# Optimization experiments

Measured on AMD Instinct MI355X. Metric: run time of the kernel, lower is better.

The kernel has to match this reference:

```python
import jax, jax.numpy as jnp
import numpy as np

DIM = 512
HEADS = 8
DIM_HEAD = 64
INNER = HEADS * DIM_HEAD  # 512


def setup_inputs() -> dict:
    key = jax.random.key(0)
    ks = jax.random.split(key, 6)
    B, N = 8, 1024
    x = jax.random.normal(ks[0], (B, N, DIM), dtype=jnp.float32)
    w_qkv = jax.random.normal(ks[1], (DIM, 3 * INNER), dtype=jnp.float32) * (DIM ** -0.5)
    reattn_weights = jax.random.normal(ks[2], (HEADS, HEADS), dtype=jnp.float32)
    ln_gamma = jnp.ones((HEADS,), dtype=jnp.float32)
    ln_beta = jnp.zeros((HEADS,), dtype=jnp.float32)
    w_out = jax.random.normal(ks[3], (INNER, DIM), dtype=jnp.float32) * (INNER ** -0.5)
    b_out = jnp.zeros((DIM,), dtype=jnp.float32)
    return {"x": x, "w_qkv": w_qkv, "reattn_weights": reattn_weights,
            "ln_gamma": ln_gamma, "ln_beta": ln_beta, "w_out": w_out, "b_out": b_out}


def reference(x, w_qkv, reattn_weights, ln_gamma, ln_beta, w_out, b_out):
    B, N, C = x.shape
    scale = DIM_HEAD ** -0.5
    qkv = (x @ w_qkv).reshape(B, N, 3, HEADS, DIM_HEAD)
    qkv = jnp.transpose(qkv, (2, 0, 3, 1, 4))  # [3, B, H, N, D]
    q, k, v = qkv[0], qkv[1], qkv[2]
    dots = jnp.einsum('bhid,bhjd->bhij', q, k) * scale
    attn = jax.nn.softmax(dots, axis=-1)
    # cross-head re-mixing
    attn = jnp.einsum('bhij,hg->bgij', attn, reattn_weights)
    # LayerNorm over the head axis per (b, i, j)
    mean = jnp.mean(attn, axis=1, keepdims=True)
    var = jnp.var(attn, axis=1, keepdims=True)
    attn = (attn - mean) * jax.lax.rsqrt(var + 1e-5)
    attn = attn * ln_gamma[None, :, None, None] + ln_beta[None, :, None, None]
    out = jnp.einsum('bhij,bhjd->bhid', attn, v)
    out = jnp.transpose(out, (0, 2, 1, 3)).reshape(B, N, INNER)
    return out @ w_out + b_out
```

## Files before the change

kernel.cpp:

```cpp
#include <hip/hip_runtime.h>
#include <hip/hip_bf16.h>
#include <stdint.h>


#define DIMC 512

typedef __attribute__((ext_vector_type(8))) short bf16x8;
typedef __attribute__((ext_vector_type(4))) float f32x4;
typedef __attribute__((ext_vector_type(8))) unsigned short u16x8;

__device__ __forceinline__ unsigned short f2bf(float f) {
    union { float f; uint32_t u; } v; v.f = f;
    uint32_t u = v.u;
    return (unsigned short)((u + 0x7fffu + ((u >> 16) & 1u)) >> 16);
}

#define MFMA(a, b, c) __builtin_amdgcn_mfma_f32_16x16x32_bf16((a), (b), (c), 0, 0, 0)

#define GLOAD16(gptr, lptr)                                                        \
    __builtin_amdgcn_global_load_lds((const __attribute__((address_space(1))) void*)(gptr), \
                                     (__attribute__((address_space(3))) void*)(lptr), 16, 0, 0)

__global__ void k_conv(const float* __restrict__ in, unsigned short* __restrict__ out, int n8) {
    int t = blockIdx.x * blockDim.x + threadIdx.x;
    if (t >= n8) return;
    const float4* p = reinterpret_cast<const float4*>(in) + (size_t)t * 2;
    float4 a = p[0], b = p[1];
    u16x8 o;
    o[0] = f2bf(a.x); o[1] = f2bf(a.y); o[2] = f2bf(a.z); o[3] = f2bf(a.w);
    o[4] = f2bf(b.x); o[5] = f2bf(b.y); o[6] = f2bf(b.z); o[7] = f2bf(b.w);
    *(reinterpret_cast<u16x8*>(out) + t) = o;
}

__global__ __launch_bounds__(256) void k_tconv(const float* __restrict__ in,
                                               unsigned short* __restrict__ out, int R, int C) {
    __shared__ float tile[64][65];
    int ct = C >> 6;
    int bx = blockIdx.x % ct;
    int by = blockIdx.x / ct;
    int r0 = by * 64, c0 = bx * 64;
    int tx = threadIdx.x & 63, ty = threadIdx.x >> 6;
#pragma unroll
    for (int rr = 0; rr < 16; rr++) {
        int row = ty + rr * 4;
        tile[row][tx] = in[(size_t)(r0 + row) * C + c0 + tx];
    }
    __syncthreads();
#pragma unroll
    for (int rr = 0; rr < 16; rr++) {
        int row = ty + rr * 4;
        out[(size_t)(c0 + row) * R + r0 + tx] = f2bf(tile[tx][row]);
    }
}

__global__ __launch_bounds__(256) void k_qkv(const unsigned short* __restrict__ A,
                                             const unsigned short* __restrict__ BT,
                                             unsigned short* __restrict__ q,
                                             unsigned short* __restrict__ kk,
                                             unsigned short* __restrict__ vv) {
    __shared__ unsigned short Al[128 * 32];
    __shared__ unsigned short Bl[128 * 32];
    int mt = blockIdx.x / 12, nt = blockIdx.x % 12;
    int m0 = mt * 128, c0 = nt * 128;
    int tid = threadIdx.x, lane = tid & 63, w = tid >> 6;
    int wr = w >> 1, wc = w & 1;
    int lr = lane & 15, lb = lane >> 4;
    f32x4 acc[4][4] = {};
    const unsigned short* gA = A + (size_t)(m0 + 32 * w + (lane >> 2)) * DIMC + (lane & 3) * 8;
    const unsigned short* gB = BT + (size_t)(c0 + 32 * w + (lane >> 2)) * DIMC + (lane & 3) * 8;
    char* lA = (char*)Al + w * 2048;
    char* lB = (char*)Bl + w * 2048;
    for (int k0 = 0; k0 < DIMC; k0 += 32) {
        __syncthreads();
        GLOAD16(gA + k0, lA);
        GLOAD16(gA + k0 + 16 * DIMC, lA + 1024);
        GLOAD16(gB + k0, lB);
        GLOAD16(gB + k0 + 16 * DIMC, lB + 1024);
        __syncthreads();
        bf16x8 af[4], bfr[4];
#pragma unroll
        for (int mi = 0; mi < 4; mi++)
            af[mi] = *reinterpret_cast<const bf16x8*>(&Al[(64 * wr + 16 * mi + lr) * 32 + 8 * lb]);
#pragma unroll
        for (int ni = 0; ni < 4; ni++)
            bfr[ni] = *reinterpret_cast<const bf16x8*>(&Bl[(64 * wc + 16 * ni + lr) * 32 + 8 * lb]);
#pragma unroll
        for (int mi = 0; mi < 4; mi++)
#pragma unroll
            for (int ni = 0; ni < 4; ni++)
                acc[mi][ni] = MFMA(af[mi], bfr[ni], acc[mi][ni]);
    }
#pragma unroll
    for (int ni = 0; ni < 4; ni++) {
        int c = c0 + 64 * wc + 16 * ni + lr;
        int which = c >> 9, rem = c & 511, h = rem >> 6, d = rem & 63;
        unsigned short* dst = which == 0 ? q : (which == 1 ? kk : vv);
        float sc = which == 0 ? 0.125f : 1.0f;
#pragma unroll
        for (int mi = 0; mi < 4; mi++) {
#pragma unroll
            for (int r = 0; r < 4; r++) {
                int m = m0 + 64 * wr + 16 * mi + 4 * lb + r;
                int b = m >> 10, n = m & 1023;
                dst[(((size_t)(b * 8 + h) * 1024) + n) * 64 + d] = f2bf(acc[mi][ni][r] * sc);
            }
        }
    }
}

__global__ __launch_bounds__(256) void k_vtrans(const unsigned short* __restrict__ v,
                                                unsigned short* __restrict__ vT) {
    __shared__ unsigned short tile[64][72];
    int bh = blockIdx.x >> 4;
    int n0 = (blockIdx.x & 15) * 64;
    int t = threadIdx.x;
    int nl = t >> 2, c4 = t & 3;
    const u16x8* src = reinterpret_cast<const u16x8*>(v + ((size_t)bh * 1024 + n0 + nl) * 64 + c4 * 16);
    u16x8 x0 = src[0], x1 = src[1];
    *reinterpret_cast<u16x8*>(&tile[nl][c4 * 16]) = x0;
    *reinterpret_cast<u16x8*>(&tile[nl][c4 * 16 + 8]) = x1;
    __syncthreads();
    int dl = t >> 2, n4 = t & 3;
#pragma unroll
    for (int c = 0; c < 2; c++) {
        u16x8 o;
#pragma unroll
        for (int i = 0; i < 8; i++) o[i] = tile[n4 * 16 + 8 * c + i][dl];
        *reinterpret_cast<u16x8*>(vT + ((size_t)bh * 64 + dl) * 1024 + n0 + n4 * 16 + 8 * c) = o;
    }
}

__global__ __launch_bounds__(512) void k_attn(const unsigned short* __restrict__ q,
                                              const unsigned short* __restrict__ kk,
                                              unsigned short* __restrict__ P) {
    __shared__ float redm[32][8];
    __shared__ float redl[32][8];
    int blk = blockIdx.x;
    int bh = blk & 63, it = blk >> 6;
    int i0 = it * 32;
    int tid = threadIdx.x, w = tid >> 6, lane = tid & 63;
    int lr = lane & 15, lb = lane >> 4;
    int j0 = w * 128;
    const unsigned short* qp = q + (size_t)bh * 65536;
    const unsigned short* kp = kk + (size_t)bh * 65536;
    bf16x8 aq[2][2];
#pragma unroll
    for (int mf = 0; mf < 2; mf++)
#pragma unroll
        for (int ks = 0; ks < 2; ks++)
            aq[mf][ks] = *reinterpret_cast<const bf16x8*>(qp + (size_t)(i0 + 16 * mf + lr) * 64 + 32 * ks + 8 * lb);
    f32x4 acc[2][8] = {};
#pragma unroll
    for (int nf = 0; nf < 8; nf++) {
#pragma unroll
        for (int ks = 0; ks < 2; ks++) {
            bf16x8 bk = *reinterpret_cast<const bf16x8*>(kp + (size_t)(j0 + 16 * nf + lr) * 64 + 32 * ks + 8 * lb);
            acc[0][nf] = MFMA(aq[0][ks], bk, acc[0][nf]);
            acc[1][nf] = MFMA(aq[1][ks], bk, acc[1][nf]);
        }
    }
    float mfin[2][4];
#pragma unroll
    for (int mf = 0; mf < 2; mf++)
#pragma unroll
        for (int r = 0; r < 4; r++) {
            float m = acc[mf][0][r];
#pragma unroll
            for (int nf = 1; nf < 8; nf++) m = fmaxf(m, acc[mf][nf][r]);
            m = fmaxf(m, __shfl_xor(m, 1)); m = fmaxf(m, __shfl_xor(m, 2));
            m = fmaxf(m, __shfl_xor(m, 4)); m = fmaxf(m, __shfl_xor(m, 8));
            mfin[mf][r] = m;
        }
    if (lr == 0) {
#pragma unroll
        for (int mf = 0; mf < 2; mf++)
#pragma unroll
            for (int r = 0; r < 4; r++) redm[16 * mf + 4 * lb + r][w] = mfin[mf][r];
    }
    __syncthreads();
#pragma unroll
    for (int mf = 0; mf < 2; mf++)
#pragma unroll
        for (int r = 0; r < 4; r++) {
            int row = 16 * mf + 4 * lb + r;
            float m = redm[row][0];
#pragma unroll
            for (int ww = 1; ww < 8; ww++) m = fmaxf(m, redm[row][ww]);
            mfin[mf][r] = m;
        }
    float lfin[2][4];
#pragma unroll
    for (int mf = 0; mf < 2; mf++)
#pragma unroll
        for (int r = 0; r < 4; r++) {
            float s = 0.f;
#pragma unroll
            for (int nf = 0; nf < 8; nf++) {
                float e = __expf(acc[mf][nf][r] - mfin[mf][r]);
                acc[mf][nf][r] = e;
                s += e;
            }
            s += __shfl_xor(s, 1); s += __shfl_xor(s, 2);
            s += __shfl_xor(s, 4); s += __shfl_xor(s, 8);
            lfin[mf][r] = s;
        }
    if (lr == 0) {
#pragma unroll
        for (int mf = 0; mf < 2; mf++)
#pragma unroll
            for (int r = 0; r < 4; r++) redl[16 * mf + 4 * lb + r][w] = lfin[mf][r];
    }
    __syncthreads();
#pragma unroll
    for (int mf = 0; mf < 2; mf++)
#pragma unroll
        for (int r = 0; r < 4; r++) {
            int row = 16 * mf + 4 * lb + r;
            float s = 0.f;
#pragma unroll
            for (int ww = 0; ww < 8; ww++) s += redl[row][ww];
            lfin[mf][r] = 1.0f / s;
        }
    unsigned short* pp = P + (size_t)bh * 1048576;
#pragma unroll
    for (int mf = 0; mf < 2; mf++)
#pragma unroll
        for (int nf = 0; nf < 8; nf++)
#pragma unroll
            for (int r = 0; r < 4; r++)
                pp[(size_t)(i0 + 16 * mf + 4 * lb + r) * 1024 + j0 + 16 * nf + lr] =
                    f2bf(acc[mf][nf][r] * lfin[mf][r]);
}

__global__ __launch_bounds__(512) void k_mixpv(const unsigned short* __restrict__ P,
                                               const unsigned short* __restrict__ vT,
                                               const float* __restrict__ Wm,
                                               const float* __restrict__ gamma,
                                               const float* __restrict__ beta,
                                               unsigned short* __restrict__ outh) {
    __shared__ unsigned short Pex[8 * 1024];
    __shared__ unsigned short PMl[8 * 1024];
    int blk = blockIdx.x;
    int b = blk & 7, it = blk >> 3;
    int i0 = it * 16;
    int tid = threadIdx.x, w = tid >> 6, lane = tid & 63;
    int lr = lane & 15, lb = lane >> 4;
    float wv[64];
#pragma unroll
    for (int x2 = 0; x2 < 64; x2++) wv[x2] = Wm[x2];
    float cv[8];
#pragma unroll
    for (int h = 0; h < 8; h++) {
        float s = 0.f;
#pragma unroll
        for (int g = 0; g < 8; g++) s += wv[h * 8 + g];
        cv[h] = s * 0.125f;
    }
    float gv[8], bvv[8];
#pragma unroll
    for (int x2 = 0; x2 < 8; x2++) { gv[x2] = gamma[x2]; bvv[x2] = beta[x2]; }
    const unsigned short* pbase = P + (size_t)(b * 8 + w) * 1048576 + (size_t)i0 * 1024;
    const unsigned short* vp = vT + (size_t)(b * 8 + w) * 65536;
    int ii = tid >> 5;
    int jj = (tid & 31) * 2;
    f32x4 accO[4] = {};

    auto PH1 = [&](int jt) {
        int j0 = jt * 64;
#pragma unroll
        for (int c = 0; c < 2; c++) {
            int o = c * 512 + lane * 8;
            GLOAD16(pbase + (size_t)(o >> 6) * 1024 + j0 + (o & 63),
                    (char*)Pex + w * 2048 + c * 1024);
        }
    };
    auto PH2 = [&]() {
        float alo[8], ahi[8];
#pragma unroll
        for (int h = 0; h < 8; h++) {
            uint32_t pv = *reinterpret_cast<const uint32_t*>(Pex + h * 1024 + ii * 64 + jj);
            alo[h] = __uint_as_float(pv << 16);
            ahi[h] = __uint_as_float(pv & 0xffff0000u);
        }
        float mgl[8], mgh[8];
        float meanl = 0.f, meanh = 0.f;
#pragma unroll
        for (int g = 0; g < 8; g++) {
            float sl = 0.f, sh = 0.f;
#pragma unroll
            for (int h = 0; h < 8; h++) { sl += alo[h] * wv[h * 8 + g]; sh += ahi[h] * wv[h * 8 + g]; }
            mgl[g] = sl; mgh[g] = sh;
        }
#pragma unroll
        for (int h = 0; h < 8; h++) { meanl += alo[h] * cv[h]; meanh += ahi[h] * cv[h]; }
        float vl = 0.f, vh = 0.f;
#pragma unroll
        for (int g = 0; g < 8; g++) {
            float dl = mgl[g] - meanl, dh = mgh[g] - meanh;
            vl += dl * dl; vh += dh * dh;
        }
        float rl = rsqrtf(vl * 0.125f + 1e-5f), rh = rsqrtf(vh * 0.125f + 1e-5f);
#pragma unroll
        for (int g = 0; g < 8; g++) {
            unsigned short ol = f2bf((mgl[g] - meanl) * rl * gv[g] + bvv[g]);
            unsigned short oh = f2bf((mgh[g] - meanh) * rh * gv[g] + bvv[g]);
            uint32_t pk = (uint32_t)ol | ((uint32_t)oh << 16);
            int byteoff = (g * 2048 + ii * 128 + jj * 2) ^ ((ii & 7) << 4);
            *reinterpret_cast<uint32_t*>((char*)PMl + byteoff) = pk;
        }
    };
    auto PH3 = [&](int jt) {
        int j0 = jt * 64;
        bf16x8 Af[2];
#pragma unroll
        for (int kc = 0; kc < 2; kc++) {
            int byteoff = (w * 2048 + lr * 128 + kc * 64 + lb * 16) ^ ((lr & 7) << 4);
            Af[kc] = *reinterpret_cast<const bf16x8*>((const char*)PMl + byteoff);
        }
#pragma unroll
        for (int kc = 0; kc < 2; kc++)
#pragma unroll
            for (int df = 0; df < 4; df++) {
                bf16x8 bv8 = *reinterpret_cast<const bf16x8*>(vp + (size_t)(16 * df + lr) * 1024 + j0 + 32 * kc + 8 * lb);
                accO[df] = MFMA(Af[kc], bv8, accO[df]);
            }
    };

    PH1(0);
    __syncthreads();
    PH2();
    __syncthreads();
    for (int jt = 0; jt < 16; jt++) {
        if (jt < 15) PH1(jt + 1);
        PH3(jt);
        __syncthreads();
        if (jt < 15) PH2();
        __syncthreads();
    }
    int bi = b * 1024 + i0;
#pragma unroll
    for (int df = 0; df < 4; df++)
#pragma unroll
        for (int r = 0; r < 4; r++)
            outh[(size_t)(bi + 4 * lb + r) * 512 + w * 64 + 16 * df + lr] = f2bf(accO[df][r]);
}

__global__ __launch_bounds__(256) void k_proj(const unsigned short* __restrict__ A,
                                              const unsigned short* __restrict__ BT,
                                              const float* __restrict__ bias,
                                              float* __restrict__ out) {
    __shared__ unsigned short Al[128 * 32];
    __shared__ unsigned short Bl[128 * 32];
    int mt = blockIdx.x >> 2, nt = blockIdx.x & 3;
    int m0 = mt * 128, c0 = nt * 128;
    int tid = threadIdx.x, lane = tid & 63, w = tid >> 6;
    int wr = w >> 1, wc = w & 1;
    int lr = lane & 15, lb = lane >> 4;
    f32x4 acc[4][4] = {};
    const unsigned short* gA = A + (size_t)(m0 + 32 * w + (lane >> 2)) * DIMC + (lane & 3) * 8;
    const unsigned short* gB = BT + (size_t)(c0 + 32 * w + (lane >> 2)) * DIMC + (lane & 3) * 8;
    char* lA = (char*)Al + w * 2048;
    char* lB = (char*)Bl + w * 2048;
    for (int k0 = 0; k0 < DIMC; k0 += 32) {
        __syncthreads();
        GLOAD16(gA + k0, lA);
        GLOAD16(gA + k0 + 16 * DIMC, lA + 1024);
        GLOAD16(gB + k0, lB);
        GLOAD16(gB + k0 + 16 * DIMC, lB + 1024);
        __syncthreads();
        bf16x8 af[4], bfr[4];
#pragma unroll
        for (int mi = 0; mi < 4; mi++)
            af[mi] = *reinterpret_cast<const bf16x8*>(&Al[(64 * wr + 16 * mi + lr) * 32 + 8 * lb]);
#pragma unroll
        for (int ni = 0; ni < 4; ni++)
            bfr[ni] = *reinterpret_cast<const bf16x8*>(&Bl[(64 * wc + 16 * ni + lr) * 32 + 8 * lb]);
#pragma unroll
        for (int mi = 0; mi < 4; mi++)
#pragma unroll
            for (int ni = 0; ni < 4; ni++)
                acc[mi][ni] = MFMA(af[mi], bfr[ni], acc[mi][ni]);
    }
#pragma unroll
    for (int ni = 0; ni < 4; ni++) {
        int c = c0 + 64 * wc + 16 * ni + lr;
        float bs = bias[c];
#pragma unroll
        for (int mi = 0; mi < 4; mi++) {
#pragma unroll
            for (int r = 0; r < 4; r++) {
                int m = m0 + 64 * wr + 16 * mi + 4 * lb + r;
                out[(size_t)m * 512 + c] = acc[mi][ni][r] + bs;
            }
        }
    }
}

extern "C" void kernel_launch(void* const* d_in, const int* in_sizes, int n_in,
                              void* d_out, int out_size, void* d_ws, size_t ws_size,
                              hipStream_t stream) {
    (void)in_sizes; (void)n_in; (void)out_size; (void)ws_size;
    const float* x      = (const float*)d_in[0];
    const float* w_qkv  = (const float*)d_in[1];
    const float* W      = (const float*)d_in[2];
    const float* gamma  = (const float*)d_in[3];
    const float* beta   = (const float*)d_in[4];
    const float* w_out  = (const float*)d_in[5];
    const float* b_out  = (const float*)d_in[6];
    float* out = (float*)d_out;

    char* ws = (char*)d_ws;
    unsigned short* xb   = (unsigned short*)(ws + 0);
    unsigned short* wbT  = (unsigned short*)(ws + 8388608);
    unsigned short* w_oT = (unsigned short*)(ws + 9961472);
    unsigned short* q    = (unsigned short*)(ws + 10485760);
    unsigned short* k    = (unsigned short*)(ws + 18874368);
    unsigned short* v    = (unsigned short*)(ws + 27262976);
    unsigned short* vT   = (unsigned short*)(ws + 35651584);
    unsigned short* outh = (unsigned short*)(ws + 44040192);
    unsigned short* P    = (unsigned short*)(ws + 52428800);

    k_conv<<<2048, 256, 0, stream>>>(x, xb, 8192 * 512 / 8);
    k_tconv<<<(512 / 64) * (1536 / 64), 256, 0, stream>>>(w_qkv, wbT, 512, 1536);
    k_tconv<<<(512 / 64) * (512 / 64), 256, 0, stream>>>(w_out, w_oT, 512, 512);
    k_qkv<<<(8192 / 128) * (1536 / 128), 256, 0, stream>>>(xb, wbT, q, k, v);
    k_vtrans<<<64 * 16, 256, 0, stream>>>(v, vT);
    k_attn<<<64 * 32, 512, 0, stream>>>(q, k, P);
    k_mixpv<<<8 * 64, 512, 0, stream>>>(P, vT, W, gamma, beta, outh);
    k_proj<<<(8192 / 128) * (512 / 128), 256, 0, stream>>>(outh, w_oT, b_out, out);
}
```

Baseline: 260.5 us.

## Halve row tiles in attention and mix kernels, stage P stores via LDS

k_attn now handles 16 query rows per block instead of 32, doubling the grid, and stages the normalized probabilities through padded shared memory so each P row is written with 16-byte vector stores instead of scattered 2-byte stores. k_mixpv now processes 8 rows per block with one element per thread and doubles its grid; its MFMA still computes 16 rows, with half the output discarded. The aim is more blocks across the CUs and coalesced writes of the large P buffer, at the cost of wasted MFMA work in the mix kernel and re-reading K and V tiles per smaller block.

```diff
diff --git a/kernel.cpp b/kernel.cpp
--- a/kernel.cpp
+++ b/kernel.cpp
@@ -133,103 +133,90 @@
 __global__ __launch_bounds__(512) void k_attn(const unsigned short* __restrict__ q,
                                               const unsigned short* __restrict__ kk,
                                               unsigned short* __restrict__ P) {
-    __shared__ float redm[32][8];
-    __shared__ float redl[32][8];
+    __shared__ float redm[16][8];
+    __shared__ float redl[16][8];
+    __shared__ unsigned short stg[8][16 * 136];
     int blk = blockIdx.x;
     int bh = blk & 63, it = blk >> 6;
-    int i0 = it * 32;
+    int i0 = it * 16;
     int tid = threadIdx.x, w = tid >> 6, lane = tid & 63;
     int lr = lane & 15, lb = lane >> 4;
     int j0 = w * 128;
     const unsigned short* qp = q + (size_t)bh * 65536;
     const unsigned short* kp = kk + (size_t)bh * 65536;
-    bf16x8 aq[2][2];
-#pragma unroll
-    for (int mf = 0; mf < 2; mf++)
-#pragma unroll
-        for (int ks = 0; ks < 2; ks++)
-            aq[mf][ks] = *reinterpret_cast<const bf16x8*>(qp + (size_t)(i0 + 16 * mf + lr) * 64 + 32 * ks + 8 * lb);
-    f32x4 acc[2][8] = {};
+    bf16x8 aq[2];
+#pragma unroll
+    for (int ks = 0; ks < 2; ks++)
+        aq[ks] = *reinterpret_cast<const bf16x8*>(qp + (size_t)(i0 + lr) * 64 + 32 * ks + 8 * lb);
+    f32x4 acc[8] = {};
 #pragma unroll
     for (int nf = 0; nf < 8; nf++) {
 #pragma unroll
         for (int ks = 0; ks < 2; ks++) {
             bf16x8 bk = *reinterpret_cast<const bf16x8*>(kp + (size_t)(j0 + 16 * nf + lr) * 64 + 32 * ks + 8 * lb);
-            acc[0][nf] = MFMA(aq[0][ks], bk, acc[0][nf]);
-            acc[1][nf] = MFMA(aq[1][ks], bk, acc[1][nf]);
-        }
-    }
-    float mfin[2][4];
-#pragma unroll
-    for (int mf = 0; mf < 2; mf++)
-#pragma unroll
-        for (int r = 0; r < 4; r++) {
-            float m = acc[mf][0][r];
-#pragma unroll
-            for (int nf = 1; nf < 8; nf++) m = fmaxf(m, acc[mf][nf][r]);
-            m = fmaxf(m, __shfl_xor(m, 1)); m = fmaxf(m, __shfl_xor(m, 2));
-            m = fmaxf(m, __shfl_xor(m, 4)); m = fmaxf(m, __shfl_xor(m, 8));
-            mfin[mf][r] = m;
-        }
+            acc[nf] = MFMA(aq[ks], bk, acc[nf]);
+        }
+    }
+    float mx[4], li[4];
+#pragma unroll
+    for (int r = 0; r < 4; r++) {
+        float m = acc[0][r];
+#pragma unroll
+        for (int nf = 1; nf < 8; nf++) m = fmaxf(m, acc[nf][r]);
+        m = fmaxf(m, __shfl_xor(m, 1)); m = fmaxf(m, __shfl_xor(m, 2));
+        m = fmaxf(m, __shfl_xor(m, 4)); m = fmaxf(m, __shfl_xor(m, 8));
+        mx[r] = m;
+    }
     if (lr == 0) {
 #pragma unroll
-        for (int mf = 0; mf < 2; mf++)
-#pragma unroll
-            for (int r = 0; r < 4; r++) redm[16 * mf + 4 * lb + r][w] = mfin[mf][r];
-    }
-    __syncthreads();
-#pragma unroll
-    for (int mf = 0; mf < 2; mf++)
-#pragma unroll
-        for (int r = 0; r < 4; r++) {
-            int row = 16 * mf + 4 * lb + r;
-            float m = redm[row][0];
-#pragma unroll
-            for (int ww = 1; ww < 8; ww++) m = fmaxf(m, redm[row][ww]);
-            mfin[mf][r] = m;
-        }
-    float lfin[2][4];
-#pragma unroll
-    for (int mf = 0; mf < 2; mf++)
-#pragma unroll
-        for (int r = 0; r < 4; r++) {
-            float s = 0.f;
-#pragma unroll
-            for (int nf = 0; nf < 8; nf++) {
-                float e = __expf(acc[mf][nf][r] - mfin[mf][r]);
-                acc[mf][nf][r] = e;
-                s += e;
-            }
-            s += __shfl_xor(s, 1); s += __shfl_xor(s, 2);
-            s += __shfl_xor(s, 4); s += __shfl_xor(s, 8);
-            lfin[mf][r] = s;
-        }
+        for (int r = 0; r < 4; r++) redm[4 * lb + r][w] = mx[r];
+    }
+    __syncthreads();
+#pragma unroll
+    for (int r = 0; r < 4; r++) {
+        float m = redm[4 * lb + r][0];
+#pragma unroll
+        for (int ww = 1; ww < 8; ww++) m = fmaxf(m, redm[4 * lb + r][ww]);
+        mx[r] = m;
+    }
+#pragma unroll
+    for (int r = 0; r < 4; r++) {
+        float s = 0.f;
+#pragma unroll
+        for (int nf = 0; nf < 8; nf++) {
+            float e = __expf(acc[nf][r] - mx[r]);
+            acc[nf][r] = e;
+            s += e;
+        }
+        s += __shfl_xor(s, 1); s += __shfl_xor(s, 2);
+        s += __shfl_xor(s, 4); s += __shfl_xor(s, 8);
+        li[r] = s;
+    }
     if (lr == 0) {
 #pragma unroll
-        for (int mf = 0; mf < 2; mf++)
-#pragma unroll
-            for (int r = 0; r < 4; r++) redl[16 * mf + 4 * lb + r][w] = lfin[mf][r];
-    }
-    __syncthreads();
-#pragma unroll
-    for (int mf = 0; mf < 2; mf++)
-#pragma unroll
-        for (int r = 0; r < 4; r++) {
-            int row = 16 * mf + 4 * lb + r;
-            float s = 0.f;
-#pragma unroll
-            for (int ww = 0; ww < 8; ww++) s += redl[row][ww];
-            lfin[mf][r] = 1.0f / s;
-        }
+        for (int r = 0; r < 4; r++) redl[4 * lb + r][w] = li[r];
+    }
+    __syncthreads();
+#pragma unroll
+    for (int r = 0; r < 4; r++) {
+        float s = 0.f;
+#pragma unroll
+        for (int ww = 0; ww < 8; ww++) s += redl[4 * lb + r][ww];
+        li[r] = 1.0f / s;
+    }
+    unsigned short* sp = &stg[w][0];
+#pragma unroll
+    for (int nf = 0; nf < 8; nf++)
+#pragma unroll
+        for (int r = 0; r < 4; r++)
+            sp[(4 * lb + r) * 136 + 16 * nf + lr] = f2bf(acc[nf][r] * li[r]);
     unsigned short* pp = P + (size_t)bh * 1048576;
 #pragma unroll
-    for (int mf = 0; mf < 2; mf++)
-#pragma unroll
-        for (int nf = 0; nf < 8; nf++)
-#pragma unroll
-            for (int r = 0; r < 4; r++)
-                pp[(size_t)(i0 + 16 * mf + 4 * lb + r) * 1024 + j0 + 16 * nf + lr] =
-                    f2bf(acc[mf][nf][r] * lfin[mf][r]);
+    for (int ss = 0; ss < 4; ss++) {
+        int rowi = 4 * ss + lb;
+        u16x8 vv = *reinterpret_cast<const u16x8*>(&stg[w][rowi * 136 + lr * 8]);
+        *reinterpret_cast<u16x8*>(pp + (size_t)(i0 + rowi) * 1024 + j0 + lr * 8) = vv;
+    }
 }
 
 __global__ __launch_bounds__(512) void k_mixpv(const unsigned short* __restrict__ P,
@@ -238,11 +225,11 @@
                                                const float* __restrict__ gamma,
                                                const float* __restrict__ beta,
                                                unsigned short* __restrict__ outh) {
-    __shared__ unsigned short Pex[8 * 1024];
+    __shared__ unsigned short Pex[8 * 512];
     __shared__ unsigned short PMl[8 * 1024];
     int blk = blockIdx.x;
     int b = blk & 7, it = blk >> 3;
-    int i0 = it * 16;
+    int i0 = it * 8;
     int tid = threadIdx.x, w = tid >> 6, lane = tid & 63;
     int lr = lane & 15, lb = lane >> 4;
     float wv[64];
@@ -259,54 +246,43 @@
     float gv[8], bvv[8];
 #pragma unroll
     for (int x2 = 0; x2 < 8; x2++) { gv[x2] = gamma[x2]; bvv[x2] = beta[x2]; }
-    const unsigned short* pbase = P + (size_t)(b * 8 + w) * 1048576 + (size_t)i0 * 1024;
     const unsigned short* vp = vT + (size_t)(b * 8 + w) * 65536;
-    int ii = tid >> 5;
-    int jj = (tid & 31) * 2;
+    int e = tid * 8;
+    int sh = e >> 9, si = (e >> 6) & 7, sj = e & 63;
+    const unsigned short* psrc = P + (size_t)(b * 8 + sh) * 1048576 + (size_t)(i0 + si) * 1024 + sj;
+    int ii = tid >> 6, jj = tid & 63;
     f32x4 accO[4] = {};
 
     auto PH1 = [&](int jt) {
-        int j0 = jt * 64;
-#pragma unroll
-        for (int c = 0; c < 2; c++) {
-            int o = c * 512 + lane * 8;
-            GLOAD16(pbase + (size_t)(o >> 6) * 1024 + j0 + (o & 63),
-                    (char*)Pex + w * 2048 + c * 1024);
-        }
+        GLOAD16(psrc + jt * 64, (char*)Pex + tid * 16);
     };
     auto PH2 = [&]() {
-        float alo[8], ahi[8];
+        float av[8];
 #pragma unroll
         for (int h = 0; h < 8; h++) {
-            uint32_t pv = *reinterpret_cast<const uint32_t*>(Pex + h * 1024 + ii * 64 + jj);
-            alo[h] = __uint_as_float(pv << 16);
-            ahi[h] = __uint_as_float(pv & 0xffff0000u);
-        }
-        float mgl[8], mgh[8];
-        float meanl = 0.f, meanh = 0.f;
+            uint32_t pv = (uint32_t)Pex[h * 512 + ii * 64 + jj];
+            av[h] = __uint_as_float(pv << 16);
+        }
+        float mg[8];
+        float mean = 0.f;
 #pragma unroll
         for (int g = 0; g < 8; g++) {
-            float sl = 0.f, sh = 0.f;
-#pragma unroll
-            for (int h = 0; h < 8; h++) { sl += alo[h] * wv[h * 8 + g]; sh += ahi[h] * wv[h * 8 + g]; }
-            mgl[g] = sl; mgh[g] = sh;
-        }
-#pragma unroll
-        for (int h = 0; h < 8; h++) { meanl += alo[h] * cv[h]; meanh += ahi[h] * cv[h]; }
-        float vl = 0.f, vh = 0.f;
+            float s = 0.f;
+#pragma unroll
+            for (int h = 0; h < 8; h++) s += av[h] * wv[h * 8 + g];
+            mg[g] = s;
+        }
+#pragma unroll
+        for (int h = 0; h < 8; h++) mean += av[h] * cv[h];
+        float vvar = 0.f;
+#pragma unroll
+        for (int g = 0; g < 8; g++) { float d = mg[g] - mean; vvar += d * d; }
+        float rs = rsqrtf(vvar * 0.125f + 1e-5f);
 #pragma unroll
         for (int g = 0; g < 8; g++) {
-            float dl = mgl[g] - meanl, dh = mgh[g] - meanh;
-            vl += dl * dl; vh += dh * dh;
-        }
-        float rl = rsqrtf(vl * 0.125f + 1e-5f), rh = rsqrtf(vh * 0.125f + 1e-5f);
-#pragma unroll
-        for (int g = 0; g < 8; g++) {
-            unsigned short ol = f2bf((mgl[g] - meanl) * rl * gv[g] + bvv[g]);
-            unsigned short oh = f2bf((mgh[g] - meanh) * rh * gv[g] + bvv[g]);
-            uint32_t pk = (uint32_t)ol | ((uint32_t)oh << 16);
+            unsigned short ov = f2bf((mg[g] - mean) * rs * gv[g] + bvv[g]);
             int byteoff = (g * 2048 + ii * 128 + jj * 2) ^ ((ii & 7) << 4);
-            *reinterpret_cast<uint32_t*>((char*)PMl + byteoff) = pk;
+            *reinterpret_cast<unsigned short*>((char*)PMl + byteoff) = ov;
         }
     };
     auto PH3 = [&](int jt) {
@@ -337,12 +313,14 @@
         if (jt < 15) PH2();
         __syncthreads();
     }
-    int bi = b * 1024 + i0;
-#pragma unroll
-    for (int df = 0; df < 4; df++)
-#pragma unroll
-        for (int r = 0; r < 4; r++)
-            outh[(size_t)(bi + 4 * lb + r) * 512 + w * 64 + 16 * df + lr] = f2bf(accO[df][r]);
+    if (lb < 2) {
+        int bi = b * 1024 + i0;
+#pragma unroll
+        for (int df = 0; df < 4; df++)
+#pragma unroll
+            for (int r = 0; r < 4; r++)
+                outh[(size_t)(bi + 4 * lb + r) * 512 + w * 64 + 16 * df + lr] = f2bf(accO[df][r]);
+    }
 }
 
 __global__ __launch_bounds__(256) void k_proj(const unsigned short* __restrict__ A,
@@ -425,7 +403,7 @@
     k_tconv<<<(512 / 64) * (512 / 64), 256, 0, stream>>>(w_out, w_oT, 512, 512);
     k_qkv<<<(8192 / 128) * (1536 / 128), 256, 0, stream>>>(xb, wbT, q, k, v);
     k_vtrans<<<64 * 16, 256, 0, stream>>>(v, vT);
-    k_attn<<<64 * 32, 512, 0, stream>>>(q, k, P);
-    k_mixpv<<<8 * 64, 512, 0, stream>>>(P, vT, W, gamma, beta, outh);
+    k_attn<<<64 * 64, 512, 0, stream>>>(q, k, P);
+    k_mixpv<<<8 * 128, 512, 0, stream>>>(P, vT, W, gamma, beta, outh);
     k_proj<<<(8192 / 128) * (512 / 128), 256, 0, stream>>>(outh, w_oT, b_out, out);
 }
```

Result: slower. 332.8 us (+27.8%).
